# Performance work log

Measured on AMD Instinct MI355X. Metric: run time of the kernel, lower is better.

## Reference

```python
import jax, jax.numpy as jnp
import numpy as np

DROPOUT_P = 0.5
LEAKY_ALPHA = 0.2
NEG_INF = -9e15


def setup_inputs() -> dict:
    key = jax.random.key(0)
    k_h, k_adj, k_W, k_a = jax.random.split(key, 4)
    B, N, F_in, F_out = 8, 2048, 128, 64
    h = jax.random.normal(k_h, (B, N, F_in), dtype=jnp.float32)
    adj = jax.random.randint(k_adj, (B, N, N), 0, 2, dtype=jnp.int32)
    W = jax.random.normal(k_W, (F_in, F_out), dtype=jnp.float32)
    a = jax.random.normal(k_a, (2 * F_out, 1), dtype=jnp.float32)
    return {"h": h, "adj": adj, "W": W, "a": a}


def reference(h, adj, W, a):
    F_out = W.shape[1]
    Wh = jnp.einsum('bni,io->bno', h, W)                 # [B,N,F_out]
    Wh1 = Wh @ a[:F_out]                                  # [B,N,1]
    Wh2 = Wh @ a[F_out:]                                  # [B,N,1]
    e = jax.nn.leaky_relu(Wh1 + jnp.swapaxes(Wh2, 1, 2), LEAKY_ALPHA)  # [B,N,N]
    att = jnp.where(adj > 0, e, NEG_INF)
    att = jax.nn.softmax(att, axis=2)
    # F.dropout(attention, 0.5) with training=True (torch default)
    keep = jax.random.bernoulli(jax.random.key(42), 1.0 - DROPOUT_P, att.shape)
    att = att * keep.astype(att.dtype) / (1.0 - DROPOUT_P)
    embedding = jnp.matmul(att, Wh)                       # [B,N,F_out]
    return embedding
```

## Files before the change

kernel.cpp:

```cpp
#include <hip/hip_runtime.h>
#include <stdint.h>

#define NB   8
#define NN   2048
#define FIN  128
#define FOUT 64
#define MAXS 512

__device__ __forceinline__ uint32_t rotl32(uint32_t x, uint32_t r) {
  return (x << r) | (x >> (32u - r));
}

__device__ __forceinline__ void threefry_0_42(uint32_t x0, uint32_t x1,
                                              uint32_t& o0, uint32_t& o1) {
  const uint32_t k0 = 0u, k1 = 42u;
  const uint32_t k2 = 0x1BD11BDAu ^ k0 ^ k1;
  x0 += k0; x1 += k1;
#define TFR(r) { x0 += x1; x1 = rotl32(x1, r); x1 ^= x0; }
  TFR(13u) TFR(15u) TFR(26u) TFR(6u)   x0 += k1; x1 += k2 + 1u;
  TFR(17u) TFR(29u) TFR(16u) TFR(24u)  x0 += k2; x1 += k0 + 2u;
  TFR(13u) TFR(15u) TFR(26u) TFR(6u)   x0 += k0; x1 += k1 + 3u;
  TFR(17u) TFR(29u) TFR(16u) TFR(24u)  x0 += k1; x1 += k2 + 4u;
  TFR(13u) TFR(15u) TFR(26u) TFR(6u)   x0 += k2; x1 += k0 + 5u;
#undef TFR
  o0 = x0; o1 = x1;
}

__device__ __forceinline__ bool keep_bit(uint32_t v) {
  uint32_t o0, o1;
  threefry_0_42(0u, v, o0, o1);
  return !((o0 ^ o1) >> 31);
}

__global__ __launch_bounds__(256) void wh_kernel(
    const float* __restrict__ h, const float* __restrict__ W,
    const float* __restrict__ a, float* __restrict__ Wh,
    float* __restrict__ Wh1, float* __restrict__ Wh2) {
  __shared__ __align__(16) float wLds[FIN * FOUT];
  __shared__ __align__(16) float hLds[16][FIN];
  const int t = threadIdx.x;
  const int wv = t >> 6, lane = t & 63;
  const int rbase = blockIdx.x * 16;
  {
    const float4* W4 = reinterpret_cast<const float4*>(W);
    float4* wL4 = reinterpret_cast<float4*>(wLds);
    for (int idx = t; idx < FIN * FOUT / 4; idx += 256) wL4[idx] = W4[idx];
    const float4* h4 = reinterpret_cast<const float4*>(h + (size_t)rbase * FIN);
    float4* hL4 = reinterpret_cast<float4*>(&hLds[0][0]);
    for (int idx = t; idx < 16 * FIN / 4; idx += 256) hL4[idx] = h4[idx];
  }
  __syncthreads();
  const int r0 = wv * 4;
  float acc0 = 0.f, acc1 = 0.f, acc2 = 0.f, acc3 = 0.f;
#pragma unroll 4
  for (int k = 0; k < FIN; ++k) {
    const float w = wLds[k * FOUT + lane];
    acc0 += hLds[r0 + 0][k] * w;
    acc1 += hLds[r0 + 1][k] * w;
    acc2 += hLds[r0 + 2][k] * w;
    acc3 += hLds[r0 + 3][k] * w;
  }
  const float a1 = a[lane], a2 = a[FOUT + lane];
  float accs[4] = {acc0, acc1, acc2, acc3};
#pragma unroll
  for (int r = 0; r < 4; ++r) {
    const int row = rbase + r0 + r;
    Wh[(size_t)row * FOUT + lane] = accs[r];
    float x1 = accs[r] * a1, x2 = accs[r] * a2;
#pragma unroll
    for (int off = 32; off >= 1; off >>= 1) {
      x1 += __shfl_xor(x1, off);
      x2 += __shfl_xor(x2, off);
    }
    if (lane == 0) { Wh1[row] = x1; Wh2[row] = x2; }
  }
}

__global__ __launch_bounds__(256) void attn_kernel(
    const int* __restrict__ adj, const float* __restrict__ Wh,
    const float* __restrict__ Wh1, const float* __restrict__ Wh2,
    float* __restrict__ out) {
  __shared__ float redA[2][4];
  __shared__ int cnt[2];
  __shared__ int   survJ[2][MAXS];
  __shared__ float survP[2][MAXS];
  __shared__ float accL[2][4][FOUT];

  const int i = blockIdx.x & (NN - 1);
  const int b = blockIdx.x >> 11;
  const int b2 = b + 4;
  const int t = threadIdx.x;
  const int wv = t >> 6, lane = t & 63;

  const float wh1_0 = Wh1[b * NN + i];
  const float wh1_1 = Wh1[b2 * NN + i];
  const size_t adjBase0 = ((size_t)(b * NN) + i) * NN;
  const size_t adjBase1 = ((size_t)(b2 * NN) + i) * NN;
  const int j0 = t * 8;

  float ww0[8], ww1[8];
  float mW0 = -3.0e38f, mW1 = -3.0e38f;
  {
    const int4   a0a = *reinterpret_cast<const int4*>(adj + adjBase0 + j0);
    const int4   a0b = *reinterpret_cast<const int4*>(adj + adjBase0 + j0 + 4);
    const int4   a1a = *reinterpret_cast<const int4*>(adj + adjBase1 + j0);
    const int4   a1b = *reinterpret_cast<const int4*>(adj + adjBase1 + j0 + 4);
    const float4 w0a = *reinterpret_cast<const float4*>(Wh2 + (size_t)b * NN + j0);
    const float4 w0b = *reinterpret_cast<const float4*>(Wh2 + (size_t)b * NN + j0 + 4);
    const float4 w1a = *reinterpret_cast<const float4*>(Wh2 + (size_t)b2 * NN + j0);
    const float4 w1b = *reinterpret_cast<const float4*>(Wh2 + (size_t)b2 * NN + j0 + 4);
    const int aa0[8] = {a0a.x, a0a.y, a0a.z, a0a.w, a0b.x, a0b.y, a0b.z, a0b.w};
    const int aa1[8] = {a1a.x, a1a.y, a1a.z, a1a.w, a1b.x, a1b.y, a1b.z, a1b.w};
    const float vv0[8] = {w0a.x, w0a.y, w0a.z, w0a.w, w0b.x, w0b.y, w0b.z, w0b.w};
    const float vv1[8] = {w1a.x, w1a.y, w1a.z, w1a.w, w1b.x, w1b.y, w1b.z, w1b.w};
#pragma unroll
    for (int e = 0; e < 8; ++e) {
      ww0[e] = (aa0[e] > 0) ? vv0[e] : -1.0e30f;
      mW0 = fmaxf(mW0, ww0[e]);
      ww1[e] = (aa1[e] > 0) ? vv1[e] : -1.0e30f;
      mW1 = fmaxf(mW1, ww1[e]);
    }
  }
#pragma unroll
  for (int off = 1; off < 64; off <<= 1) {
    mW0 = fmaxf(mW0, __shfl_xor(mW0, off));
    mW1 = fmaxf(mW1, __shfl_xor(mW1, off));
  }
  if (lane == 0) { redA[0][wv] = mW0; redA[1][wv] = mW1; }
  if (t < 2) cnt[t] = 0;
  __syncthreads();
  mW0 = fmaxf(fmaxf(redA[0][0], redA[0][1]), fmaxf(redA[0][2], redA[0][3]));
  mW1 = fmaxf(fmaxf(redA[1][0], redA[1][1]), fmaxf(redA[1][2], redA[1][3]));

  const float me0_arg = wh1_0 + mW0;
  const float me1_arg = wh1_1 + mW1;
  const float me0 = (me0_arg < 0.f) ? 0.2f * me0_arg : me0_arg;
  const float me1 = (me1_arg < 0.f) ? 0.2f * me1_arg : me1_arg;
  const float thr0 = mW0 - 116.f;
  const float thr1 = mW1 - 116.f;

  float s0 = 0.f, s1 = 0.f;
#pragma unroll
  for (int k = 0; k < 8; ++k) {
    if (ww0[k] > thr0) {
      float x = wh1_0 + ww0[k];
      x = (x < 0.f) ? 0.2f * x : x;
      const float p = __expf(x - me0);
      s0 += p;
      if (p > 1e-10f) {
        const int idx = atomicAdd(&cnt[0], 1);
        if (idx < MAXS) { survJ[0][idx] = j0 + k; survP[0][idx] = p; }
      }
    }
    if (ww1[k] > thr1) {
      float y = wh1_1 + ww1[k];
      y = (y < 0.f) ? 0.2f * y : y;
      const float p = __expf(y - me1);
      s1 += p;
      if (p > 1e-10f) {
        const int idx = atomicAdd(&cnt[1], 1);
        if (idx < MAXS) { survJ[1][idx] = j0 + k; survP[1][idx] = p; }
      }
    }
  }
#pragma unroll
  for (int off = 1; off < 64; off <<= 1) {
    s0 += __shfl_xor(s0, off);
    s1 += __shfl_xor(s1, off);
  }
  if (lane == 0) { redA[0][wv] = s0; redA[1][wv] = s1; }
  __syncthreads();
  s0 = redA[0][0] + redA[0][1] + redA[0][2] + redA[0][3];
  s1 = redA[1][0] + redA[1][1] + redA[1][2] + redA[1][3];
  const float inv0 = 2.0f / s0;
  const float inv1 = 2.0f / s1;
  const int c0 = min(cnt[0], MAXS), c1 = min(cnt[1], MAXS);

  for (int idx = t; idx < c0; idx += 256) {
    const uint32_t v = ((uint32_t)b << 22) | ((uint32_t)i << 11) | (uint32_t)survJ[0][idx];
    survP[0][idx] = keep_bit(v) ? survP[0][idx] * inv0 : 0.f;
  }
  for (int idx = t; idx < c1; idx += 256) {
    const uint32_t v = ((uint32_t)b2 << 22) | ((uint32_t)i << 11) | (uint32_t)survJ[1][idx];
    survP[1][idx] = keep_bit(v) ? survP[1][idx] * inv1 : 0.f;
  }
  __syncthreads();

  float acc0 = 0.f, acc1 = 0.f;
  for (int idx = wv; idx < c0; idx += 4) {
    const float c = survP[0][idx];
    if (c != 0.f)
      acc0 += c * Wh[((size_t)(b * NN + survJ[0][idx])) * FOUT + lane];
  }
  for (int idx = wv; idx < c1; idx += 4) {
    const float c = survP[1][idx];
    if (c != 0.f)
      acc1 += c * Wh[((size_t)(b2 * NN + survJ[1][idx])) * FOUT + lane];
  }
  accL[0][wv][lane] = acc0;
  accL[1][wv][lane] = acc1;
  __syncthreads();
  if (t < 128) {
    const int bb = t >> 6, f = t & 63;
    const float r = accL[bb][0][f] + accL[bb][1][f] + accL[bb][2][f] + accL[bb][3][f];
    const int bo = (bb == 0) ? b : b2;
    out[((size_t)bo * NN + i) * FOUT + f] = r;
  }
}

extern "C" void kernel_launch(void* const* d_in, const int* in_sizes, int n_in,
                              void* d_out, int out_size, void* d_ws, size_t ws_size,
                              hipStream_t stream) {
  const float* h   = (const float*)d_in[0];
  const int*   adj = (const int*)d_in[1];
  const float* W   = (const float*)d_in[2];
  const float* a   = (const float*)d_in[3];
  float* out = (float*)d_out;
  float* ws  = (float*)d_ws;

  float* Wh  = ws;
  float* Wh1 = ws + (size_t)NB * NN * FOUT;
  float* Wh2 = Wh1 + NB * NN;

  wh_kernel<<<dim3((NB * NN) / 16), dim3(256), 0, stream>>>(h, W, a, Wh, Wh1, Wh2);
  attn_kernel<<<dim3((NB / 2) * NN), dim3(256), 0, stream>>>(adj, Wh, Wh1, Wh2, out);
}
```

Measured before the change: 51.16 us.

## Map one attention row per wavefront with ballot-driven survivor gathering

Restructures the attention kernel so that each wavefront handles one full output row, with 4 rows per block, instead of each block handling two rows from different batches. All max and sum reductions become wave-local shuffles, so shared memory, LDS atomics and block barriers are no longer needed. Survivors are found with a ballot and iterated per wave, applying the dropout hash inline before the Wh gather. The survivor compaction and the MAXS cap go away, so the result is exact. The risk is a serial per-survivor loop with shuffles inside a single wave, and the threshold prefilter that skipped exp for masked entries is gone.

```diff
diff --git a/kernel.cpp b/kernel.cpp
--- a/kernel.cpp
+++ b/kernel.cpp
@@ -5,7 +5,6 @@
 #define NN   2048
 #define FIN  128
 #define FOUT 64
-#define MAXS 512
 
 __device__ __forceinline__ uint32_t rotl32(uint32_t x, uint32_t r) {
   return (x << r) | (x >> (32u - r));
@@ -80,132 +79,68 @@
     const int* __restrict__ adj, const float* __restrict__ Wh,
     const float* __restrict__ Wh1, const float* __restrict__ Wh2,
     float* __restrict__ out) {
-  __shared__ float redA[2][4];
-  __shared__ int cnt[2];
-  __shared__ int   survJ[2][MAXS];
-  __shared__ float survP[2][MAXS];
-  __shared__ float accL[2][4][FOUT];
-
-  const int i = blockIdx.x & (NN - 1);
-  const int b = blockIdx.x >> 11;
-  const int b2 = b + 4;
   const int t = threadIdx.x;
   const int wv = t >> 6, lane = t & 63;
+  const int r = blockIdx.x * 4 + wv;
+  const int b = r >> 11;
 
-  const float wh1_0 = Wh1[b * NN + i];
-  const float wh1_1 = Wh1[b2 * NN + i];
-  const size_t adjBase0 = ((size_t)(b * NN) + i) * NN;
-  const size_t adjBase1 = ((size_t)(b2 * NN) + i) * NN;
-  const int j0 = t * 8;
+  const float wh1 = Wh1[r];
+  const int4*   adjv = reinterpret_cast<const int4*>(adj) + (size_t)r * (NN / 4);
+  const float4* wh2v = reinterpret_cast<const float4*>(Wh2) + (size_t)b * (NN / 4);
 
-  float ww0[8], ww1[8];
-  float mW0 = -3.0e38f, mW1 = -3.0e38f;
-  {
-    const int4   a0a = *reinterpret_cast<const int4*>(adj + adjBase0 + j0);
-    const int4   a0b = *reinterpret_cast<const int4*>(adj + adjBase0 + j0 + 4);
-    const int4   a1a = *reinterpret_cast<const int4*>(adj + adjBase1 + j0);
-    const int4   a1b = *reinterpret_cast<const int4*>(adj + adjBase1 + j0 + 4);
-    const float4 w0a = *reinterpret_cast<const float4*>(Wh2 + (size_t)b * NN + j0);
-    const float4 w0b = *reinterpret_cast<const float4*>(Wh2 + (size_t)b * NN + j0 + 4);
-    const float4 w1a = *reinterpret_cast<const float4*>(Wh2 + (size_t)b2 * NN + j0);
-    const float4 w1b = *reinterpret_cast<const float4*>(Wh2 + (size_t)b2 * NN + j0 + 4);
-    const int aa0[8] = {a0a.x, a0a.y, a0a.z, a0a.w, a0b.x, a0b.y, a0b.z, a0b.w};
-    const int aa1[8] = {a1a.x, a1a.y, a1a.z, a1a.w, a1b.x, a1b.y, a1b.z, a1b.w};
-    const float vv0[8] = {w0a.x, w0a.y, w0a.z, w0a.w, w0b.x, w0b.y, w0b.z, w0b.w};
-    const float vv1[8] = {w1a.x, w1a.y, w1a.z, w1a.w, w1b.x, w1b.y, w1b.z, w1b.w};
+  float pv[8][4];
+  float mW = -3.0e38f;
 #pragma unroll
-    for (int e = 0; e < 8; ++e) {
-      ww0[e] = (aa0[e] > 0) ? vv0[e] : -1.0e30f;
-      mW0 = fmaxf(mW0, ww0[e]);
-      ww1[e] = (aa1[e] > 0) ? vv1[e] : -1.0e30f;
-      mW1 = fmaxf(mW1, ww1[e]);
+  for (int c = 0; c < 8; ++c) {
+    const int4   av = adjv[c * 64 + lane];
+    const float4 w2 = wh2v[c * 64 + lane];
+    pv[c][0] = (av.x > 0) ? w2.x : -1.0e30f;
+    pv[c][1] = (av.y > 0) ? w2.y : -1.0e30f;
+    pv[c][2] = (av.z > 0) ? w2.z : -1.0e30f;
+    pv[c][3] = (av.w > 0) ? w2.w : -1.0e30f;
+    mW = fmaxf(mW, fmaxf(fmaxf(pv[c][0], pv[c][1]), fmaxf(pv[c][2], pv[c][3])));
+  }
+#pragma unroll
+  for (int off = 1; off < 64; off <<= 1) mW = fmaxf(mW, __shfl_xor(mW, off));
+
+  const float me_arg = wh1 + mW;
+  const float me = (me_arg < 0.f) ? 0.2f * me_arg : me_arg;
+
+  float s = 0.f;
+#pragma unroll
+  for (int c = 0; c < 8; ++c) {
+#pragma unroll
+    for (int e = 0; e < 4; ++e) {
+      float z = wh1 + pv[c][e];
+      z = (z < 0.f) ? 0.2f * z : z;
+      const float p = __expf(z - me);
+      s += p;
+      pv[c][e] = p;
     }
   }
 #pragma unroll
-  for (int off = 1; off < 64; off <<= 1) {
-    mW0 = fmaxf(mW0, __shfl_xor(mW0, off));
-    mW1 = fmaxf(mW1, __shfl_xor(mW1, off));
-  }
-  if (lane == 0) { redA[0][wv] = mW0; redA[1][wv] = mW1; }
-  if (t < 2) cnt[t] = 0;
-  __syncthreads();
-  mW0 = fmaxf(fmaxf(redA[0][0], redA[0][1]), fmaxf(redA[0][2], redA[0][3]));
-  mW1 = fmaxf(fmaxf(redA[1][0], redA[1][1]), fmaxf(redA[1][2], redA[1][3]));
+  for (int off = 1; off < 64; off <<= 1) s += __shfl_xor(s, off);
+  const float inv = 2.0f / s;
 
-  const float me0_arg = wh1_0 + mW0;
-  const float me1_arg = wh1_1 + mW1;
-  const float me0 = (me0_arg < 0.f) ? 0.2f * me0_arg : me0_arg;
-  const float me1 = (me1_arg < 0.f) ? 0.2f * me1_arg : me1_arg;
-  const float thr0 = mW0 - 116.f;
-  const float thr1 = mW1 - 116.f;
-
-  float s0 = 0.f, s1 = 0.f;
+  float acc = 0.f;
+  const uint32_t vbase = (uint32_t)r << 11;
 #pragma unroll
-  for (int k = 0; k < 8; ++k) {
-    if (ww0[k] > thr0) {
-      float x = wh1_0 + ww0[k];
-      x = (x < 0.f) ? 0.2f * x : x;
-      const float p = __expf(x - me0);
-      s0 += p;
-      if (p > 1e-10f) {
-        const int idx = atomicAdd(&cnt[0], 1);
-        if (idx < MAXS) { survJ[0][idx] = j0 + k; survP[0][idx] = p; }
-      }
-    }
-    if (ww1[k] > thr1) {
-      float y = wh1_1 + ww1[k];
-      y = (y < 0.f) ? 0.2f * y : y;
-      const float p = __expf(y - me1);
-      s1 += p;
-      if (p > 1e-10f) {
-        const int idx = atomicAdd(&cnt[1], 1);
-        if (idx < MAXS) { survJ[1][idx] = j0 + k; survP[1][idx] = p; }
+  for (int c = 0; c < 8; ++c) {
+#pragma unroll
+    for (int e = 0; e < 4; ++e) {
+      unsigned long long msk = __ballot(pv[c][e] > 1e-10f);
+      while (msk) {
+        const int src = __builtin_ctzll(msk);
+        msk &= msk - 1;
+        const int j = c * 256 + src * 4 + e;
+        if (keep_bit(vbase | (uint32_t)j)) {
+          const float cc = __shfl(pv[c][e], src) * inv;
+          acc += cc * Wh[((size_t)(b * NN + j)) * FOUT + lane];
+        }
       }
     }
   }
-#pragma unroll
-  for (int off = 1; off < 64; off <<= 1) {
-    s0 += __shfl_xor(s0, off);
-    s1 += __shfl_xor(s1, off);
-  }
-  if (lane == 0) { redA[0][wv] = s0; redA[1][wv] = s1; }
-  __syncthreads();
-  s0 = redA[0][0] + redA[0][1] + redA[0][2] + redA[0][3];
-  s1 = redA[1][0] + redA[1][1] + redA[1][2] + redA[1][3];
-  const float inv0 = 2.0f / s0;
-  const float inv1 = 2.0f / s1;
-  const int c0 = min(cnt[0], MAXS), c1 = min(cnt[1], MAXS);
-
-  for (int idx = t; idx < c0; idx += 256) {
-    const uint32_t v = ((uint32_t)b << 22) | ((uint32_t)i << 11) | (uint32_t)survJ[0][idx];
-    survP[0][idx] = keep_bit(v) ? survP[0][idx] * inv0 : 0.f;
-  }
-  for (int idx = t; idx < c1; idx += 256) {
-    const uint32_t v = ((uint32_t)b2 << 22) | ((uint32_t)i << 11) | (uint32_t)survJ[1][idx];
-    survP[1][idx] = keep_bit(v) ? survP[1][idx] * inv1 : 0.f;
-  }
-  __syncthreads();
-
-  float acc0 = 0.f, acc1 = 0.f;
-  for (int idx = wv; idx < c0; idx += 4) {
-    const float c = survP[0][idx];
-    if (c != 0.f)
-      acc0 += c * Wh[((size_t)(b * NN + survJ[0][idx])) * FOUT + lane];
-  }
-  for (int idx = wv; idx < c1; idx += 4) {
-    const float c = survP[1][idx];
-    if (c != 0.f)
-      acc1 += c * Wh[((size_t)(b2 * NN + survJ[1][idx])) * FOUT + lane];
-  }
-  accL[0][wv][lane] = acc0;
-  accL[1][wv][lane] = acc1;
-  __syncthreads();
-  if (t < 128) {
-    const int bb = t >> 6, f = t & 63;
-    const float r = accL[bb][0][f] + accL[bb][1][f] + accL[bb][2][f] + accL[bb][3][f];
-    const int bo = (bb == 0) ? b : b2;
-    out[((size_t)bo * NN + i) * FOUT + f] = r;
-  }
+  out[(size_t)r * FOUT + lane] = acc;
 }
 
 extern "C" void kernel_launch(void* const* d_in, const int* in_sizes, int n_in,
@@ -223,5 +158,5 @@
   float* Wh2 = Wh1 + NB * NN;
 
   wh_kernel<<<dim3((NB * NN) / 16), dim3(256), 0, stream>>>(h, W, a, Wh, Wh1, Wh2);
-  attn_kernel<<<dim3((NB / 2) * NN), dim3(256), 0, stream>>>(adj, Wh, Wh1, Wh2, out);
+  attn_kernel<<<dim3((NB * NN) / 4), dim3(256), 0, stream>>>(adj, Wh, Wh1, Wh2, out);
 }
```

New measurement: 86.68 us. 1.69x slower.
